# Kernel tuning notes

Hardware: AMD Instinct MI355X
Metric: run time of the kernel (lower is better)

Reference implementation:

```python
import jax, jax.numpy as jnp
import numpy as np

N = 50000      # nodes
M = 800000     # edges
D = 128        # node_state_dim == msg_dim
EF = 32        # edge_feat_dim
DF = 32        # node_dist_feat_dim
ATT = 128      # att_hidden_dim
L = 2          # num_layer (num_prop = 1)
IN = D + EF + DF  # 192, MLP input dim


def setup_inputs() -> dict:
    key = jax.random.key(0)
    ks = jax.random.split(key, 18)
    rn = lambda k, shape, s=0.05: jax.random.normal(k, shape, dtype=jnp.float32) * s
    return {
        "node_feat":   rn(ks[0], (N, D), 1.0),
        "node_feat_c": rn(ks[1], (N, D), 1.0),
        "edge":        jax.random.randint(ks[2], (M, 2), 0, N, dtype=jnp.int32),
        "edge_feat":   rn(ks[3], (M, EF), 1.0),
        "dist_feat":   rn(ks[4], (M, DF), 1.0),
        # msg MLP: Linear(IN->D) -> ReLU -> Linear(D->D), stacked over layers
        "msg_w0": rn(ks[5], (L, IN, D)),  "msg_b0": jnp.zeros((L, D), jnp.float32),
        "msg_w1": rn(ks[6], (L, D, D)),   "msg_b1": jnp.zeros((L, D), jnp.float32),
        # attention head: Linear(IN->ATT) -> ReLU -> Linear(ATT->D) -> Sigmoid
        "att_w0": rn(ks[7], (L, IN, ATT)), "att_b0": jnp.zeros((L, ATT), jnp.float32),
        "att_w1": rn(ks[8], (L, ATT, D)),  "att_b1": jnp.zeros((L, D), jnp.float32),
        # LSTMCell params (torch layout: W_ih [4H, in], W_hh [4H, H], gate order i,f,g,o)
        "lstm_wih": rn(ks[9],  (L, 4 * D, D)),
        "lstm_whh": rn(ks[10], (L, 4 * D, D)),
        "lstm_bih": jnp.zeros((L, 4 * D), jnp.float32),
        "lstm_bhh": jnp.zeros((L, 4 * D), jnp.float32),
    }


def _lstm_cell(x, h, c, wih, whh, bih, bhh):
    gates = x @ wih.T + bih + h @ whh.T + bhh          # [N, 4D]
    i, f, g, o = jnp.split(gates, 4, axis=1)
    c2 = jax.nn.sigmoid(f) * c + jax.nn.sigmoid(i) * jnp.tanh(g)
    h2 = jax.nn.sigmoid(o) * jnp.tanh(c2)
    return h2, c2


def reference(node_feat, node_feat_c, edge, edge_feat, dist_feat,
              msg_w0, msg_b0, msg_w1, msg_b1,
              att_w0, att_b0, att_w1, att_b1,
              lstm_wih, lstm_whh, lstm_bih, lstm_bhh):
    src = edge[:, 0]
    dst = edge[:, 1]
    state, state_c = node_feat, node_feat_c
    for ii in range(L):
        if ii > 0:
            state = jax.nn.relu(state)
        # _prop (num_prop = 1)
        state_diff = state[src] - state[dst]                               # [M, D]
        edge_input = jnp.concatenate([state_diff, edge_feat, dist_feat], 1)  # [M, IN]
        msg = jax.nn.relu(edge_input @ msg_w0[ii] + msg_b0[ii]) @ msg_w1[ii] + msg_b1[ii]
        att = jax.nn.sigmoid(
            jax.nn.relu(edge_input @ att_w0[ii] + att_b0[ii]) @ att_w1[ii] + att_b1[ii])
        msg = msg * att
        state_msg = jax.ops.segment_sum(msg, dst, num_segments=N)          # scatter_add
        state, state_c = _lstm_cell(state_msg, state, state_c,
                                    lstm_wih[ii], lstm_whh[ii],
                                    lstm_bih[ii], lstm_bhh[ii])
    return state
```

## Files before the change

kernel.cpp:

```cpp
#include <hip/hip_runtime.h>
#include <hip/hip_bf16.h>

constexpr int N  = 50000;
constexpr int M  = 800000;
constexpr int D  = 128;
constexpr int IN = 192;
constexpr int TE = 128;
constexpr int NCH = 20;
constexpr int NBLK = (N + 255) / 256;

typedef __attribute__((ext_vector_type(4)))  short short4v;
typedef __attribute__((ext_vector_type(8)))  short short8;
typedef __attribute__((ext_vector_type(16))) float f32x16;

__device__ __align__(16) short g_wp[163840];
__device__ __align__(16) short g_lw[262144];
__device__ __align__(16) short g_efdf[(size_t)M * 64];
__device__ __align__(16) short g_sbf[(size_t)N * D];
__device__ int g_cnt[N];
__device__ int g_part[NBLK];
__device__ int g_ssrc[M];
__device__ int g_sdst[M];
__device__ int g_inv[M];

__device__ __forceinline__ float sigm(float x) { return 1.0f / (1.0f + __expf(-x)); }

__device__ __forceinline__ short f2bf(float f) {
    unsigned u = __builtin_bit_cast(unsigned, f);
    u = (u + 0x7FFFu + ((u >> 16) & 1u)) >> 16;
    return (short)u;
}
__device__ __forceinline__ float bf2f(short s) {
    return __builtin_bit_cast(float, ((unsigned)(unsigned short)s) << 16);
}
__device__ __forceinline__ unsigned pk2(float a, float b) {
    __hip_bfloat162 h = __float22bfloat162_rn(float2{a, b});
    unsigned u;
    __builtin_memcpy(&u, &h, 4);
    return u;
}

__global__ void zero_cnt_kernel() {
    for (int i = blockIdx.x * 256 + threadIdx.x; i < N; i += gridDim.x * 256) g_cnt[i] = 0;
}
__global__ void hist_kernel(const int* __restrict__ edge) {
    int e = blockIdx.x * 256 + threadIdx.x;
    if (e < M) atomicAdd(&g_cnt[edge[e * 2 + 1]], 1);
}
__global__ void scanA_kernel() {
    __shared__ int red[256];
    const int t = threadIdx.x;
    const int idx = blockIdx.x * 256 + t;
    red[t] = (idx < N) ? g_cnt[idx] : 0;
    __syncthreads();
#pragma unroll
    for (int s = 128; s > 0; s >>= 1) {
        if (t < s) red[t] += red[t + s];
        __syncthreads();
    }
    if (t == 0) g_part[blockIdx.x] = red[0];
}
__global__ void scanB_kernel() {
    __shared__ int sh[256];
    const int t = threadIdx.x;
    int v = (t < NBLK) ? g_part[t] : 0;
    sh[t] = v;
    __syncthreads();
    int x = v;
    for (int s = 1; s < 256; s <<= 1) {
        int y = (t >= s) ? sh[t - s] : 0;
        __syncthreads();
        x += y; sh[t] = x;
        __syncthreads();
    }
    if (t < NBLK) g_part[t] = x - v;
}
__global__ void scanC_kernel() {
    __shared__ int sh[256];
    const int t = threadIdx.x;
    const int idx = blockIdx.x * 256 + t;
    int v = (idx < N) ? g_cnt[idx] : 0;
    sh[t] = v;
    __syncthreads();
    int x = v;
    for (int s = 1; s < 256; s <<= 1) {
        int y = (t >= s) ? sh[t - s] : 0;
        __syncthreads();
        x += y; sh[t] = x;
        __syncthreads();
    }
    if (idx < N) g_cnt[idx] = g_part[blockIdx.x] + x - v;
}
__global__ void scatter_kernel(const int* __restrict__ edge) {
    int e = blockIdx.x * 256 + threadIdx.x;
    if (e < M) {
        const int s = edge[e * 2], d = edge[e * 2 + 1];
        const int p = atomicAdd(&g_cnt[d], 1);
        g_ssrc[p] = s;
        g_sdst[p] = d;
        g_inv[p]  = e;
    }
}

__global__ void pack_edge(const float* __restrict__ w0m, const float* __restrict__ w0a,
                          const float* __restrict__ w1m, const float* __restrict__ w1a) {
    int gid = blockIdx.x * 256 + threadIdx.x;
    int ii = gid / 81920;
    int r  = gid % 81920;
    int p  = r / 40960;  r %= 40960;
    int which = (r >= 24576) ? 1 : 0;
    int r2 = which ? r - 24576 : r;
    int e    = r2 & 7;
    int f    = r2 >> 3;
    int lane = f & 63;
    int ktct = f >> 6;
    int ct = ktct & 3, kt = ktct >> 2;
    int k   = kt * 16 + ((lane >> 5) << 3) + e;
    int col = ct * 32 + (lane & 31);
    const float* w0 = p ? w0a : w0m;
    const float* w1 = p ? w1a : w1m;
    float v = which ? w1[((size_t)ii * D + k) * D + col]
                    : w0[((size_t)ii * IN + k) * D + col];
    g_wp[gid] = f2bf(v);
}

__global__ void pack_lstm(const float* __restrict__ wih, const float* __restrict__ whh) {
    int gid = blockIdx.x * 256 + threadIdx.x;
    int ii = gid >> 17;
    int r  = gid & 131071;
    int e = r & 7, f = r >> 3;
    int lane = f & 63, rest = f >> 6;
    int cf = rest & 15, kt = rest >> 4;
    int col = cf * 32 + (lane & 31);
    int k   = (kt & 7) * 16 + ((lane >> 5) << 3) + e;
    const float* src = (kt < 8) ? wih : whh;
    g_lw[gid] = f2bf(src[((size_t)ii * 512 + col) * D + k]);
}

__global__ void pack_efdf(const float* __restrict__ ef, const float* __restrict__ df) {
    int gid = blockIdx.x * 256 + threadIdx.x;
    int p = gid >> 3, c0 = (gid & 7) * 8;
    const int e = g_inv[p];
    const float* s = (c0 < 32) ? (ef + (size_t)e * 32 + c0) : (df + (size_t)e * 32 + (c0 - 32));
    float4 u0 = *(const float4*)s, u1 = *(const float4*)(s + 4);
    short8 t;
    unsigned* tp = (unsigned*)&t;
    tp[0] = pk2(u0.x, u0.y); tp[1] = pk2(u0.z, u0.w);
    tp[2] = pk2(u1.x, u1.y); tp[3] = pk2(u1.z, u1.w);
    *(short8*)(g_efdf + (size_t)gid * 8) = t;
}

__global__ void init_kernel(const float4* __restrict__ nf, const float4* __restrict__ nfc,
                            float4* __restrict__ state, float4* __restrict__ state_c) {
    const int total = N * D / 4;
    for (int i = blockIdx.x * blockDim.x + threadIdx.x; i < total; i += gridDim.x * blockDim.x) {
        state[i]   = nf[i];
        state_c[i] = nfc[i];
    }
}

__global__ void prep_kernel(float4* __restrict__ state, float4* __restrict__ msg, int do_relu) {
    const int total = N * D / 4;
    const float4 z = make_float4(0.f, 0.f, 0.f, 0.f);
    for (int i = blockIdx.x * blockDim.x + threadIdx.x; i < total; i += gridDim.x * blockDim.x) {
        float4 v = state[i];
        if (do_relu) {
            v.x = fmaxf(v.x, 0.f); v.y = fmaxf(v.y, 0.f);
            v.z = fmaxf(v.z, 0.f); v.w = fmaxf(v.w, 0.f);
            state[i] = v;
        }
        short4v b;
        unsigned* bp = (unsigned*)&b;
        bp[0] = pk2(v.x, v.y); bp[1] = pk2(v.z, v.w);
        *(short4v*)(g_sbf + (size_t)i * 4) = b;
        msg[i] = z;
    }
}

#define MFMA(a, b, c) __builtin_amdgcn_mfma_f32_32x32x16_bf16(a, b, c, 0, 0, 0)

template<int BASE>
__device__ __forceinline__ void gemmA(const short8* __restrict__ gsrc, short8* wb,
                                      const short8 a1[12], int tid, int lane, int cg,
                                      f32x16& o0, f32x16& o1) {
    f32x16 acc0 = {}, acc1 = {};
#pragma unroll
    for (int c = 0; c < 6; ++c) {
        const int gc = BASE + c;
        short8 g;
        if (gc + 1 < NCH) g = gsrc[(size_t)(gc + 1) * 512 + tid];
        const short8* buf = wb + (gc & 1) * 512;
#pragma unroll
        for (int kl = 0; kl < 2; ++kl) {
            short8 b0 = buf[(kl * 4 + cg * 2 + 0) * 64 + lane];
            short8 b1 = buf[(kl * 4 + cg * 2 + 1) * 64 + lane];
            acc0 = MFMA(a1[c * 2 + kl], b0, acc0);
            acc1 = MFMA(a1[c * 2 + kl], b1, acc1);
        }
        if (gc + 1 < NCH) wb[((gc + 1) & 1) * 512 + tid] = g;
        __syncthreads();
    }
    o0 = acc0; o1 = acc1;
}

template<int BASE>
__device__ __forceinline__ void gemmH(const short8* __restrict__ gsrc, short8* wb,
                                      const short (*hsr)[136], int tid, int lane, int cg, int half,
                                      f32x16& o0, f32x16& o1) {
    f32x16 acc0 = {}, acc1 = {};
#pragma unroll
    for (int c = 0; c < 4; ++c) {
        const int gc = BASE + c;
        short8 g;
        if (gc + 1 < NCH) g = gsrc[(size_t)(gc + 1) * 512 + tid];
        const short8* buf = wb + (gc & 1) * 512;
#pragma unroll
        for (int kl = 0; kl < 2; ++kl) {
            const int kt = c * 2 + kl;
            short8 a2 = *(const short8*)&hsr[lane & 31][kt * 16 + half];
            short8 b0 = buf[(kl * 4 + cg * 2 + 0) * 64 + lane];
            short8 b1 = buf[(kl * 4 + cg * 2 + 1) * 64 + lane];
            acc0 = MFMA(a2, b0, acc0);
            acc1 = MFMA(a2, b1, acc1);
        }
        if (gc + 1 < NCH) wb[((gc + 1) & 1) * 512 + tid] = g;
        __syncthreads();
    }
    o0 = acc0; o1 = acc1;
}

__device__ __forceinline__ void hwrite(short (*hsr)[136], const f32x16& a0, const f32x16& a1v,
                                       const float* __restrict__ b0, int lane, int cg) {
#pragma unroll
    for (int ct = 0; ct < 2; ++ct) {
        const int col = cg * 64 + ct * 32 + (lane & 31);
        const float bv = b0[col];
        f32x16 a = ct ? a1v : a0;
#pragma unroll
        for (int rp = 0; rp < 8; ++rp) {
            const int reg = rp * 2;
            const int row = (reg & 3) + 8 * (reg >> 2) + 4 * (lane >> 5);
            const unsigned pr = pk2(fmaxf(a[reg] + bv, 0.f), fmaxf(a[reg + 1] + bv, 0.f));
            hsr[row][col]     = (short)(pr & 0xFFFF);
            hsr[row + 1][col] = (short)(pr >> 16);
        }
    }
}

__global__ __launch_bounds__(512, 4)
void edge_mfma(int ii,
               const float* __restrict__ b0m, const float* __restrict__ b1m,
               const float* __restrict__ b0a, const float* __restrict__ b1a,
               float* __restrict__ state_msg) {
    __shared__ __align__(16) char pool[51712];
    short8* wb = (short8*)pool;
    short (*hs)[32][136] = (short(*)[32][136])(pool + 16384);
    int* sdst = (int*)(pool + 51200);

    const int tid  = threadIdx.x;
    const int lane = tid & 63;
    const int w    = tid >> 6;
    const int rt   = w >> 1;
    const int cg   = w & 1;
    const int e0   = blockIdx.x * TE;

    if (tid < TE) sdst[tid] = g_sdst[e0 + tid];

    const int er   = e0 + rt * 32 + (lane & 31);
    const int half = (lane >> 5) << 3;
    const int s  = g_ssrc[er];
    const int d2 = g_sdst[er];
    const short* srow = g_sbf + (size_t)s  * D;
    const short* drow = g_sbf + (size_t)d2 * D;
    short8 a1[12];
#pragma unroll
    for (int kt = 0; kt < 8; ++kt) {
        const int k0 = kt * 16 + half;
        short8 sv = *(const short8*)(srow + k0);
        short8 dv = *(const short8*)(drow + k0);
        short8 t;
        unsigned* tp = (unsigned*)&t;
#pragma unroll
        for (int i = 0; i < 4; ++i)
            tp[i] = pk2(bf2f(sv[2 * i])     - bf2f(dv[2 * i]),
                        bf2f(sv[2 * i + 1]) - bf2f(dv[2 * i + 1]));
        a1[kt] = t;
    }
#pragma unroll
    for (int kt = 8; kt < 12; ++kt)
        a1[kt] = *(const short8*)(g_efdf + (size_t)er * 64 + (kt - 8) * 16 + half);

    const short8* gsrc = (const short8*)(g_wp + (size_t)ii * 81920);

    wb[tid] = gsrc[tid];
    __syncthreads();

    f32x16 t0, t1, m0, m1, c0, c1;
    gemmA<0>(gsrc, wb, a1, tid, lane, cg, t0, t1);
    hwrite(hs[rt], t0, t1, b0m, lane, cg);
    __syncthreads();
    gemmH<6>(gsrc, wb, hs[rt], tid, lane, cg, half, m0, m1);

    unsigned mb[16];
#pragma unroll
    for (int ct = 0; ct < 2; ++ct) {
        const float bm = b1m[cg * 64 + ct * 32 + (lane & 31)];
        f32x16 mv = ct ? m1 : m0;
#pragma unroll
        for (int rp = 0; rp < 8; ++rp)
            mb[ct * 8 + rp] = pk2(mv[rp * 2] + bm, mv[rp * 2 + 1] + bm);
    }

    gemmA<10>(gsrc, wb, a1, tid, lane, cg, t0, t1);
    hwrite(hs[rt], t0, t1, b0a, lane, cg);
    __syncthreads();
    gemmH<16>(gsrc, wb, hs[rt], tid, lane, cg, half, c0, c1);

    float (*vt)[132] = (float(*)[132])pool;
    const int colr = tid & 127;
    const int sub  = tid >> 7;
#pragma unroll
    for (int pass = 0; pass < 2; ++pass) {
        if ((rt >> 1) == pass) {
#pragma unroll
            for (int ct = 0; ct < 2; ++ct) {
                const int col = cg * 64 + ct * 32 + (lane & 31);
                const float ba = b1a[col];
                f32x16 av = ct ? c1 : c0;
#pragma unroll
                for (int rp = 0; rp < 8; ++rp) {
                    const int reg = rp * 2;
                    const unsigned u = mb[ct * 8 + rp];
                    const int row = (rt & 1) * 32 + (reg & 3) + 8 * (reg >> 2) + 4 * (lane >> 5);
                    vt[row][col]     = bf2f((short)(u & 0xFFFF)) * sigm(av[reg] + ba);
                    vt[row + 1][col] = bf2f((short)(u >> 16))    * sigm(av[reg + 1] + ba);
                }
            }
        }
        __syncthreads();
        const int gbase = pass * 64 + sub * 16;
        float run = 0.f;
        int cur = sdst[gbase];
#pragma unroll 4
        for (int r = 0; r < 16; ++r) {
            const int dd = sdst[gbase + r];
            if (dd != cur) {
                atomicAdd(state_msg + (size_t)cur * D + colr, run);
                run = 0.f; cur = dd;
            }
            run += vt[sub * 16 + r][colr];
        }
        atomicAdd(state_msg + (size_t)cur * D + colr, run);
        __syncthreads();
    }
}

__global__ __launch_bounds__(256, 4)
void lstm_mfma(const float* __restrict__ x, float* __restrict__ hbuf, float* __restrict__ cbuf,
               int ii,
               const float* __restrict__ bih, const float* __restrict__ bhh) {
    __shared__ short8 wb[2048];
    const int tid  = threadIdx.x;
    const int lane = tid & 63;
    const int w    = tid >> 6;
    const int n0   = blockIdx.x * 32;
    const int half = (lane >> 5) << 3;
    const int nl   = lane & 31;
    const int nld  = min(n0 + nl, N - 1);

    const short8* gsrc = (const short8*)(g_lw + (size_t)ii * 131072);

    {
        short8 g[4];
#pragma unroll
        for (int i = 0; i < 4; ++i) g[i] = gsrc[tid + i * 256];
#pragma unroll
        for (int i = 0; i < 4; ++i) wb[tid + i * 256] = g[i];
        __syncthreads();
    }

    f32x16 acc[4] = {};
#pragma unroll
    for (int kt = 0; kt < 16; ++kt) {
        const float* srow = (kt < 8) ? (x + (size_t)nld * D + kt * 16 + half)
                                     : (hbuf + (size_t)nld * D + (kt - 8) * 16 + half);
        float4 u0 = *(const float4*)(srow);
        float4 u1 = *(const float4*)(srow + 4);
        short8 a;
        unsigned* ap = (unsigned*)&a;
        ap[0] = pk2(u0.x, u0.y); ap[1] = pk2(u0.z, u0.w);
        ap[2] = pk2(u1.x, u1.y); ap[3] = pk2(u1.z, u1.w);

        short8 g[4];
        if (kt + 1 < 16) {
            const short8* p = gsrc + (size_t)(kt + 1) * 1024;
#pragma unroll
            for (int i = 0; i < 4; ++i) g[i] = p[tid + i * 256];
        }
        const short8* buf = wb + (kt & 1) * 1024;
#pragma unroll
        for (int q = 0; q < 4; ++q) {
            short8 b = buf[(q * 4 + w) * 64 + lane];
            acc[q] = MFMA(a, b, acc[q]);
        }
        if (kt + 1 < 16) {
            short8* d = wb + ((kt + 1) & 1) * 1024;
#pragma unroll
            for (int i = 0; i < 4; ++i) d[tid + i * 256] = g[i];
        }
        __syncthreads();
    }

    const int col = (w << 5) + nl;
    const float bi = bih[col]       + bhh[col];
    const float bf = bih[128 + col] + bhh[128 + col];
    const float bg = bih[256 + col] + bhh[256 + col];
    const float bo = bih[384 + col] + bhh[384 + col];
#pragma unroll
    for (int reg = 0; reg < 16; ++reg) {
        const int nn = (reg & 3) + 8 * (reg >> 2) + 4 * (lane >> 5);
        const int n = n0 + nn;
        if (n < N) {
            const float gi = acc[0][reg] + bi;
            const float gf = acc[1][reg] + bf;
            const float gg = acc[2][reg] + bg;
            const float go = acc[3][reg] + bo;
            float* cp = cbuf + (size_t)n * D + col;
            const float c2 = sigm(gf) * (*cp) + sigm(gi) * tanhf(gg);
            const float h2 = sigm(go) * tanhf(c2);
            *cp = c2;
            hbuf[(size_t)n * D + col] = h2;
        }
    }
}

extern "C" void kernel_launch(void* const* d_in, const int* in_sizes, int n_in,
                              void* d_out, int out_size, void* d_ws, size_t ws_size,
                              hipStream_t stream) {
    const float* node_feat   = (const float*)d_in[0];
    const float* node_feat_c = (const float*)d_in[1];
    const int*   edge        = (const int*)d_in[2];
    const float* edge_feat   = (const float*)d_in[3];
    const float* dist_feat   = (const float*)d_in[4];
    const float* msg_w0 = (const float*)d_in[5];
    const float* msg_b0 = (const float*)d_in[6];
    const float* msg_w1 = (const float*)d_in[7];
    const float* msg_b1 = (const float*)d_in[8];
    const float* att_w0 = (const float*)d_in[9];
    const float* att_b0 = (const float*)d_in[10];
    const float* att_w1 = (const float*)d_in[11];
    const float* att_b1 = (const float*)d_in[12];
    const float* lstm_wih = (const float*)d_in[13];
    const float* lstm_whh = (const float*)d_in[14];
    const float* lstm_bih = (const float*)d_in[15];
    const float* lstm_bhh = (const float*)d_in[16];

    float* state     = (float*)d_out;
    float* state_c   = (float*)d_ws;
    float* state_msg = (float*)d_ws + (size_t)N * D;

    zero_cnt_kernel<<<256, 256, 0, stream>>>();
    hist_kernel<<<(M + 255) / 256, 256, 0, stream>>>(edge);
    scanA_kernel<<<NBLK, 256, 0, stream>>>();
    scanB_kernel<<<1, 256, 0, stream>>>();
    scanC_kernel<<<NBLK, 256, 0, stream>>>();
    scatter_kernel<<<(M + 255) / 256, 256, 0, stream>>>(edge);

    pack_efdf<<<25000, 256, 0, stream>>>(edge_feat, dist_feat);
    pack_edge<<<640, 256, 0, stream>>>(msg_w0, att_w0, msg_w1, att_w1);
    pack_lstm<<<1024, 256, 0, stream>>>(lstm_wih, lstm_whh);

    init_kernel<<<2048, 256, 0, stream>>>((const float4*)node_feat, (const float4*)node_feat_c,
                                          (float4*)state, (float4*)state_c);

    for (int ii = 0; ii < 2; ++ii) {
        prep_kernel<<<2048, 256, 0, stream>>>((float4*)state, (float4*)state_msg, ii > 0 ? 1 : 0);

        edge_mfma<<<M / TE, 512, 0, stream>>>(
            ii,
            msg_b0 + (size_t)ii * D, msg_b1 + (size_t)ii * D,
            att_b0 + (size_t)ii * D, att_b1 + (size_t)ii * D,
            state_msg);

        lstm_mfma<<<(N + 31) / 32, 256, 0, stream>>>(
            state_msg, state, state_c, ii,
            lstm_bih + (size_t)ii * 4 * D, lstm_bhh + (size_t)ii * 4 * D);
    }
}
```

Measured before the change: 914.7 us.

## Switch edge MLP to fp16 MFMA and double weight chunk size

Edge-MLP weights, edge features and bf16 node state are now packed as fp16 and multiplied with the f16 MFMA. The state difference becomes a packed half-vector subtraction, replacing per-element bf16 unpack/repack. Weight staging chunks double in size (10 chunks instead of 20), which halves the barrier count but raises LDS use per block and may lower occupancy. fp16 has narrower range than bf16, and the round-toward-zero packing adds some numeric risk.

```diff
diff --git a/kernel.cpp b/kernel.cpp
--- a/kernel.cpp
+++ b/kernel.cpp
@@ -6,12 +6,13 @@
 constexpr int D  = 128;
 constexpr int IN = 192;
 constexpr int TE = 128;
-constexpr int NCH = 20;
+constexpr int NCH = 10;
 constexpr int NBLK = (N + 255) / 256;
 
 typedef __attribute__((ext_vector_type(4)))  short short4v;
 typedef __attribute__((ext_vector_type(8)))  short short8;
 typedef __attribute__((ext_vector_type(16))) float f32x16;
+typedef _Float16 half8  __attribute__((ext_vector_type(8)));
 
 __device__ __align__(16) short g_wp[163840];
 __device__ __align__(16) short g_lw[262144];
@@ -30,14 +31,25 @@
     u = (u + 0x7FFFu + ((u >> 16) & 1u)) >> 16;
     return (short)u;
 }
-__device__ __forceinline__ float bf2f(short s) {
-    return __builtin_bit_cast(float, ((unsigned)(unsigned short)s) << 16);
-}
 __device__ __forceinline__ unsigned pk2(float a, float b) {
     __hip_bfloat162 h = __float22bfloat162_rn(float2{a, b});
     unsigned u;
     __builtin_memcpy(&u, &h, 4);
     return u;
+}
+__device__ __forceinline__ unsigned pkh(float a, float b) {
+    auto h = __builtin_amdgcn_cvt_pkrtz(a, b);
+    unsigned u;
+    __builtin_memcpy(&u, &h, 4);
+    return u;
+}
+__device__ __forceinline__ short f2h(float f) {
+    _Float16 h = (_Float16)f;
+    return __builtin_bit_cast(short, h);
+}
+__device__ __forceinline__ float h2f(short s) {
+    _Float16 h = __builtin_bit_cast(_Float16, s);
+    return (float)h;
 }
 
 __global__ void zero_cnt_kernel() {
@@ -121,7 +133,7 @@
     const float* w1 = p ? w1a : w1m;
     float v = which ? w1[((size_t)ii * D + k) * D + col]
                     : w0[((size_t)ii * IN + k) * D + col];
-    g_wp[gid] = f2bf(v);
+    g_wp[gid] = f2h(v);
 }
 
 __global__ void pack_lstm(const float* __restrict__ wih, const float* __restrict__ whh) {
@@ -145,8 +157,8 @@
     float4 u0 = *(const float4*)s, u1 = *(const float4*)(s + 4);
     short8 t;
     unsigned* tp = (unsigned*)&t;
-    tp[0] = pk2(u0.x, u0.y); tp[1] = pk2(u0.z, u0.w);
-    tp[2] = pk2(u1.x, u1.y); tp[3] = pk2(u1.z, u1.w);
+    tp[0] = pkh(u0.x, u0.y); tp[1] = pkh(u0.z, u0.w);
+    tp[2] = pkh(u1.x, u1.y); tp[3] = pkh(u1.z, u1.w);
     *(short8*)(g_efdf + (size_t)gid * 8) = t;
 }
 
@@ -171,59 +183,72 @@
         }
         short4v b;
         unsigned* bp = (unsigned*)&b;
-        bp[0] = pk2(v.x, v.y); bp[1] = pk2(v.z, v.w);
+        bp[0] = pkh(v.x, v.y); bp[1] = pkh(v.z, v.w);
         *(short4v*)(g_sbf + (size_t)i * 4) = b;
         msg[i] = z;
     }
 }
 
-#define MFMA(a, b, c) __builtin_amdgcn_mfma_f32_32x32x16_bf16(a, b, c, 0, 0, 0)
-
-template<int BASE>
+#define MFMA16(a, b, c) __builtin_amdgcn_mfma_f32_32x32x16_f16(a, b, c, 0, 0, 0)
+#define MFMABF(a, b, c) __builtin_amdgcn_mfma_f32_32x32x16_bf16(a, b, c, 0, 0, 0)
+
+template<int BASE, int NC>
 __device__ __forceinline__ void gemmA(const short8* __restrict__ gsrc, short8* wb,
-                                      const short8 a1[12], int tid, int lane, int cg,
+                                      const half8 a1[12], int tid, int lane, int cg,
                                       f32x16& o0, f32x16& o1) {
     f32x16 acc0 = {}, acc1 = {};
 #pragma unroll
-    for (int c = 0; c < 6; ++c) {
+    for (int c = 0; c < NC; ++c) {
         const int gc = BASE + c;
-        short8 g;
-        if (gc + 1 < NCH) g = gsrc[(size_t)(gc + 1) * 512 + tid];
-        const short8* buf = wb + (gc & 1) * 512;
-#pragma unroll
-        for (int kl = 0; kl < 2; ++kl) {
-            short8 b0 = buf[(kl * 4 + cg * 2 + 0) * 64 + lane];
-            short8 b1 = buf[(kl * 4 + cg * 2 + 1) * 64 + lane];
-            acc0 = MFMA(a1[c * 2 + kl], b0, acc0);
-            acc1 = MFMA(a1[c * 2 + kl], b1, acc1);
-        }
-        if (gc + 1 < NCH) wb[((gc + 1) & 1) * 512 + tid] = g;
+        short8 g0, g1;
+        if (gc + 1 < NCH) {
+            g0 = gsrc[(size_t)(gc + 1) * 1024 + tid];
+            g1 = gsrc[(size_t)(gc + 1) * 1024 + tid + 512];
+        }
+        const short8* buf = wb + (gc & 1) * 1024;
+#pragma unroll
+        for (int kl = 0; kl < 4; ++kl) {
+            half8 b0 = __builtin_bit_cast(half8, buf[(kl * 4 + cg * 2 + 0) * 64 + lane]);
+            half8 b1 = __builtin_bit_cast(half8, buf[(kl * 4 + cg * 2 + 1) * 64 + lane]);
+            acc0 = MFMA16(a1[c * 4 + kl], b0, acc0);
+            acc1 = MFMA16(a1[c * 4 + kl], b1, acc1);
+        }
+        if (gc + 1 < NCH) {
+            short8* d = wb + ((gc + 1) & 1) * 1024;
+            d[tid] = g0; d[tid + 512] = g1;
+        }
         __syncthreads();
     }
     o0 = acc0; o1 = acc1;
 }
 
-template<int BASE>
+template<int BASE, int NC>
 __device__ __forceinline__ void gemmH(const short8* __restrict__ gsrc, short8* wb,
                                       const short (*hsr)[136], int tid, int lane, int cg, int half,
                                       f32x16& o0, f32x16& o1) {
     f32x16 acc0 = {}, acc1 = {};
 #pragma unroll
-    for (int c = 0; c < 4; ++c) {
+    for (int c = 0; c < NC; ++c) {
         const int gc = BASE + c;
-        short8 g;
-        if (gc + 1 < NCH) g = gsrc[(size_t)(gc + 1) * 512 + tid];
-        const short8* buf = wb + (gc & 1) * 512;
-#pragma unroll
-        for (int kl = 0; kl < 2; ++kl) {
-            const int kt = c * 2 + kl;
-            short8 a2 = *(const short8*)&hsr[lane & 31][kt * 16 + half];
-            short8 b0 = buf[(kl * 4 + cg * 2 + 0) * 64 + lane];
-            short8 b1 = buf[(kl * 4 + cg * 2 + 1) * 64 + lane];
-            acc0 = MFMA(a2, b0, acc0);
-            acc1 = MFMA(a2, b1, acc1);
-        }
-        if (gc + 1 < NCH) wb[((gc + 1) & 1) * 512 + tid] = g;
+        short8 g0, g1;
+        if (gc + 1 < NCH) {
+            g0 = gsrc[(size_t)(gc + 1) * 1024 + tid];
+            g1 = gsrc[(size_t)(gc + 1) * 1024 + tid + 512];
+        }
+        const short8* buf = wb + (gc & 1) * 1024;
+#pragma unroll
+        for (int kl = 0; kl < 4; ++kl) {
+            const int kt = c * 4 + kl;
+            half8 a2 = __builtin_bit_cast(half8, *(const short8*)&hsr[lane & 31][kt * 16 + half]);
+            half8 b0 = __builtin_bit_cast(half8, buf[(kl * 4 + cg * 2 + 0) * 64 + lane]);
+            half8 b1 = __builtin_bit_cast(half8, buf[(kl * 4 + cg * 2 + 1) * 64 + lane]);
+            acc0 = MFMA16(a2, b0, acc0);
+            acc1 = MFMA16(a2, b1, acc1);
+        }
+        if (gc + 1 < NCH) {
+            short8* d = wb + ((gc + 1) & 1) * 1024;
+            d[tid] = g0; d[tid + 512] = g1;
+        }
         __syncthreads();
     }
     o0 = acc0; o1 = acc1;
@@ -240,7 +265,7 @@
         for (int rp = 0; rp < 8; ++rp) {
             const int reg = rp * 2;
             const int row = (reg & 3) + 8 * (reg >> 2) + 4 * (lane >> 5);
-            const unsigned pr = pk2(fmaxf(a[reg] + bv, 0.f), fmaxf(a[reg + 1] + bv, 0.f));
+            const unsigned pr = pkh(fmaxf(a[reg] + bv, 0.f), fmaxf(a[reg + 1] + bv, 0.f));
             hsr[row][col]     = (short)(pr & 0xFFFF);
             hsr[row + 1][col] = (short)(pr >> 16);
         }
@@ -252,10 +277,10 @@
                const float* __restrict__ b0m, const float* __restrict__ b1m,
                const float* __restrict__ b0a, const float* __restrict__ b1a,
                float* __restrict__ state_msg) {
-    __shared__ __align__(16) char pool[51712];
+    __shared__ __align__(16) char pool[68096];
     short8* wb = (short8*)pool;
-    short (*hs)[32][136] = (short(*)[32][136])(pool + 16384);
-    int* sdst = (int*)(pool + 51200);
+    short (*hs)[32][136] = (short(*)[32][136])(pool + 32768);
+    int* sdst = (int*)(pool + 67584);
 
     const int tid  = threadIdx.x;
     const int lane = tid & 63;
@@ -272,34 +297,29 @@
     const int d2 = g_sdst[er];
     const short* srow = g_sbf + (size_t)s  * D;
     const short* drow = g_sbf + (size_t)d2 * D;
-    short8 a1[12];
+    half8 a1[12];
 #pragma unroll
     for (int kt = 0; kt < 8; ++kt) {
         const int k0 = kt * 16 + half;
-        short8 sv = *(const short8*)(srow + k0);
-        short8 dv = *(const short8*)(drow + k0);
-        short8 t;
-        unsigned* tp = (unsigned*)&t;
-#pragma unroll
-        for (int i = 0; i < 4; ++i)
-            tp[i] = pk2(bf2f(sv[2 * i])     - bf2f(dv[2 * i]),
-                        bf2f(sv[2 * i + 1]) - bf2f(dv[2 * i + 1]));
-        a1[kt] = t;
+        half8 sv = __builtin_bit_cast(half8, *(const short8*)(srow + k0));
+        half8 dv = __builtin_bit_cast(half8, *(const short8*)(drow + k0));
+        a1[kt] = sv - dv;
     }
 #pragma unroll
     for (int kt = 8; kt < 12; ++kt)
-        a1[kt] = *(const short8*)(g_efdf + (size_t)er * 64 + (kt - 8) * 16 + half);
+        a1[kt] = __builtin_bit_cast(half8, *(const short8*)(g_efdf + (size_t)er * 64 + (kt - 8) * 16 + half));
 
     const short8* gsrc = (const short8*)(g_wp + (size_t)ii * 81920);
 
     wb[tid] = gsrc[tid];
+    wb[tid + 512] = gsrc[tid + 512];
     __syncthreads();
 
     f32x16 t0, t1, m0, m1, c0, c1;
-    gemmA<0>(gsrc, wb, a1, tid, lane, cg, t0, t1);
+    gemmA<0, 3>(gsrc, wb, a1, tid, lane, cg, t0, t1);
     hwrite(hs[rt], t0, t1, b0m, lane, cg);
     __syncthreads();
-    gemmH<6>(gsrc, wb, hs[rt], tid, lane, cg, half, m0, m1);
+    gemmH<3, 2>(gsrc, wb, hs[rt], tid, lane, cg, half, m0, m1);
 
     unsigned mb[16];
 #pragma unroll
@@ -308,13 +328,13 @@
         f32x16 mv = ct ? m1 : m0;
 #pragma unroll
         for (int rp = 0; rp < 8; ++rp)
-            mb[ct * 8 + rp] = pk2(mv[rp * 2] + bm, mv[rp * 2 + 1] + bm);
-    }
-
-    gemmA<10>(gsrc, wb, a1, tid, lane, cg, t0, t1);
+            mb[ct * 8 + rp] = pkh(mv[rp * 2] + bm, mv[rp * 2 + 1] + bm);
+    }
+
+    gemmA<5, 3>(gsrc, wb, a1, tid, lane, cg, t0, t1);
     hwrite(hs[rt], t0, t1, b0a, lane, cg);
     __syncthreads();
-    gemmH<16>(gsrc, wb, hs[rt], tid, lane, cg, half, c0, c1);
+    gemmH<8, 2>(gsrc, wb, hs[rt], tid, lane, cg, half, c0, c1);
 
     float (*vt)[132] = (float(*)[132])pool;
     const int colr = tid & 127;
@@ -332,8 +352,8 @@
                     const int reg = rp * 2;
                     const unsigned u = mb[ct * 8 + rp];
                     const int row = (rt & 1) * 32 + (reg & 3) + 8 * (reg >> 2) + 4 * (lane >> 5);
-                    vt[row][col]     = bf2f((short)(u & 0xFFFF)) * sigm(av[reg] + ba);
-                    vt[row + 1][col] = bf2f((short)(u >> 16))    * sigm(av[reg + 1] + ba);
+                    vt[row][col]     = h2f((short)(u & 0xFFFF)) * sigm(av[reg] + ba);
+                    vt[row + 1][col] = h2f((short)(u >> 16))    * sigm(av[reg + 1] + ba);
                 }
             }
         }
@@ -401,7 +421,7 @@
 #pragma unroll
         for (int q = 0; q < 4; ++q) {
             short8 b = buf[(q * 4 + w) * 64 + lane];
-            acc[q] = MFMA(a, b, acc[q]);
+            acc[q] = MFMABF(a, b, acc[q]);
         }
         if (kt + 1 < 16) {
             short8* d = wb + ((kt + 1) & 1) * 1024;
```

Result: faster. 887.8 us (-2.9%).
